# Performance work log

Hardware: AMD Instinct MI355X
Metric: run time of the kernel (lower is better)

The kernel has to match this reference:

```python
import jax, jax.numpy as jnp
import numpy as np

NUM_BINS = 23
SIGMA_RATIO = 0.5
SMOOTH_NR = 1e-07
SMOOTH_DR = 1e-07

BIN_CENTERS = jnp.linspace(0.0, 1.0, NUM_BINS)  # [bins]
_sigma = jnp.mean(BIN_CENTERS[1:] - BIN_CENTERS[:-1]) * SIGMA_RATIO
PRETERM = 1.0 / (2.0 * _sigma ** 2)


def setup_inputs() -> dict:
    key = jax.random.key(0)
    k1, k2 = jax.random.split(key)
    shape = (4, 1, 96, 96, 96)
    pred = jax.random.uniform(k1, shape, dtype=jnp.float32)
    target = jax.random.uniform(k2, shape, dtype=jnp.float32)
    return {"pred": pred, "target": target}


def _parzen(img):
    # img: [B, ...] -> weight [B, N, bins], probability [B, 1, bins]
    img = jnp.clip(img, 0.0, 1.0)
    img = img.reshape(img.shape[0], -1, 1)  # [B, N, 1]
    weight = jnp.exp(-PRETERM * (img - BIN_CENTERS[None, None, :]) ** 2)  # [B, N, bins]
    weight = weight / jnp.sum(weight, axis=-1, keepdims=True)
    probability = jnp.mean(weight, axis=-2, keepdims=True)  # [B, 1, bins]
    return weight, probability


def reference(pred, target):
    wa, pa = _parzen(pred)    # wa: [B, N, bins]
    wb, pb = _parzen(target)
    n = wa.shape[1]
    # joint histogram: [B, bins, bins]
    pab = jnp.einsum('bni,bnj->bij', wa, wb) / n
    # marginal product: [B, bins, bins]
    papb = jnp.einsum('bki,bkj->bij', pa, pb)
    mi = jnp.sum(pab * jnp.log((pab + SMOOTH_NR) / (papb + SMOOTH_DR) + SMOOTH_DR), axis=(1, 2))
    return -jnp.mean(mi)
```

## Files before the change

kernel.cpp:

```cpp
#include <hip/hip_runtime.h>
#include <math.h>


#define NBINS   23
#define NCELLS  529
#define NBATCH  4
#define NVOX    884736
#define PBLK    432
#define RPB     16
#define RBLK    (PBLK / RPB)
#define RS      72
#define IMGB    (32 * RS * 2)
#define WREG    (2 * IMGB)

typedef float    vf4  __attribute__((ext_vector_type(4)));
typedef _Float16 h8   __attribute__((ext_vector_type(8)));
typedef float    f16v __attribute__((ext_vector_type(16)));

#define G1 0.13533528f
#define G2 3.3546263e-4f
#define G3 1.5229979e-8f

__device__ __forceinline__ float window7(float x, int& i0, float* w)
{
    x = fminf(fmaxf(x, 0.0f), 1.0f);
    int ka = (int)floorf(fmaf(x, 22.0f, 0.5f));
    i0 = min(max(ka - 3, 0), 16);
    float v  = fmaf((float)(i0 + 3), -(1.0f / 22.0f), x);
    float W0 = __expf(-968.0f * v * v);
    float R  = __expf(88.0f * v);
    float Ri = __builtin_amdgcn_rcpf(R);
    float R2 = R * R,   R3 = R2 * R;
    float R2i = Ri * Ri, R3i = R2i * Ri;
    w[0] = W0 * (R3i * G3);
    w[1] = W0 * (R2i * G2);
    w[2] = W0 * (Ri  * G1);
    w[3] = W0;
    w[4] = W0 * (R   * G1);
    w[5] = W0 * (R2  * G2);
    w[6] = W0 * (R3  * G3);
    return ((w[0] + w[6]) + (w[1] + w[5])) + ((w[2] + w[4]) + w[3]);
}

__global__ __launch_bounds__(256)
void mi_mfma(const float* __restrict__ pred,
             const float* __restrict__ targ,
             float* __restrict__ partial)
{
    __shared__ __align__(16) char smem[4 * WREG];

    const int p    = blockIdx.x;
    const int b    = blockIdx.y;
    const int wv   = threadIdx.x >> 6;
    const int lane = threadIdx.x & 63;
    const int m    = lane & 31;
    const int h    = lane >> 5;

    char* wbase = smem + wv * WREG;
    _Float16* Aimg = (_Float16*)wbase;
    _Float16* Bimg = (_Float16*)(wbase + IMGB);

    const size_t base = (size_t)b * NVOX + (size_t)p * 2048 + (size_t)wv * 512
                      + (size_t)lane * 8;
    const vf4* __restrict__ px4 = (const vf4*)(pred + base);
    const vf4* __restrict__ py4 = (const vf4*)(targ + base);
    vf4 xa = px4[0], xb = px4[1], ya = py4[0], yb = py4[1];
    float xs[8] = {xa.x, xa.y, xa.z, xa.w, xb.x, xb.y, xb.z, xb.w};
    float ys[8] = {ya.x, ya.y, ya.z, ya.w, yb.x, yb.y, yb.z, yb.w};

    f16v acc = {};

    #pragma unroll
    for (int c = 0; c < 8; ++c) {
        vf4 z = {0.f, 0.f, 0.f, 0.f};
        #pragma unroll
        for (int it = 0; it < 3; ++it) {
            *(vf4*)(wbase        + (it * 64 + lane) * 16) = z;
            *(vf4*)(wbase + IMGB + (it * 64 + lane) * 16) = z;
        }
        if (lane < 24) {
            *(vf4*)(wbase        + (192 + lane) * 16) = z;
            *(vf4*)(wbase + IMGB + (192 + lane) * 16) = z;
        }

        int ia, ja;
        float wa[7], wb[7];
        float sa = window7(xs[c], ia, wa);
        float sb = window7(ys[c], ja, wb);
        float inv = __builtin_amdgcn_rcpf(sa * sb);

        #pragma unroll
        for (int t = 0; t < 7; ++t) {
            Aimg[(ia + t) * RS + lane] = (_Float16)(wa[t] * inv);
            Bimg[(ja + t) * RS + lane] = (_Float16)wb[t];
        }

        #pragma unroll
        for (int s = 0; s < 4; ++s) {
            h8 Af = *(const h8*)(Aimg + m * RS + 16 * s + 8 * h);
            h8 Bf = *(const h8*)(Bimg + m * RS + 16 * s + 8 * h);
            acc = __builtin_amdgcn_mfma_f32_32x32x16_f16(Af, Bf, acc, 0, 0, 0);
        }
    }

    float* tile = (float*)wbase;
    #pragma unroll
    for (int r = 0; r < 16; ++r) {
        int row = (r & 3) + 8 * (r >> 2) + 4 * h;
        tile[row * 33 + m] = acc[r];
    }
    __syncthreads();
    for (int c = threadIdx.x; c < NCELLS; c += 256) {
        int i = c / NBINS, j = c % NBINS;
        float s = 0.0f;
        #pragma unroll
        for (int w = 0; w < 4; ++w)
            s += ((const float*)(smem + w * WREG))[i * 33 + j];
        partial[((size_t)(b * PBLK + p)) * NCELLS + c] = s;
    }
}

__global__ __launch_bounds__(256)
void mi_reduce(const float* __restrict__ partial, double* __restrict__ pab64)
{
    const int g = blockIdx.x;
    const int b = blockIdx.y;
    const int t = threadIdx.x;
    const float* __restrict__ src =
        partial + ((size_t)b * PBLK + (size_t)g * RPB) * NCELLS;

    double a0 = 0.0, a1 = 0.0, a2 = 0.0;
    #pragma unroll
    for (int p = 0; p < RPB; ++p) {
        const float* __restrict__ row = src + (size_t)p * NCELLS;
        a0 += (double)row[t];
        a1 += (double)row[256 + t];
        if (t < NCELLS - 512) a2 += (double)row[512 + t];
    }
    atomicAdd(&pab64[b * NCELLS + t],       a0);
    atomicAdd(&pab64[b * NCELLS + 256 + t], a1);
    if (t < NCELLS - 512) atomicAdd(&pab64[b * NCELLS + 512 + t], a2);
}

__global__ __launch_bounds__(256)
void mi_final(const double* __restrict__ pab64, float* __restrict__ out)
{
    __shared__ double s_pab[NCELLS];
    __shared__ double s_pa[NBINS];
    __shared__ double s_pb[NBINS];
    __shared__ double s_red[4];

    double total = 0.0;
    for (int b = 0; b < NBATCH; ++b) {
        for (int c = threadIdx.x; c < NCELLS; c += 256)
            s_pab[c] = pab64[b * NCELLS + c] * (1.0 / (double)NVOX);
        __syncthreads();
        if (threadIdx.x < NBINS) {
            const int i = threadIdx.x;
            double r = 0.0, cl = 0.0;
            for (int j = 0; j < NBINS; ++j) {
                r  += s_pab[i * NBINS + j];
                cl += s_pab[j * NBINS + i];
            }
            s_pa[i] = r; s_pb[i] = cl;
        }
        __syncthreads();
        double t = 0.0;
        for (int c = threadIdx.x; c < NCELLS; c += 256) {
            double pv   = s_pab[c];
            double papb = s_pa[c / NBINS] * s_pb[c % NBINS];
            t += pv * log((pv + 1e-7) / (papb + 1e-7) + 1e-7);
        }
        #pragma unroll
        for (int off = 32; off > 0; off >>= 1) t += __shfl_down(t, off, 64);
        if ((threadIdx.x & 63) == 0) s_red[threadIdx.x >> 6] = t;
        __syncthreads();
        if (threadIdx.x == 0) total += s_red[0] + s_red[1] + s_red[2] + s_red[3];
        __syncthreads();
    }
    if (threadIdx.x == 0) out[0] = (float)(-total * 0.25);
}

extern "C" void kernel_launch(void* const* d_in, const int* in_sizes, int n_in,
                              void* d_out, int out_size, void* d_ws, size_t ws_size,
                              hipStream_t stream)
{
    const float* pred = (const float*)d_in[0];
    const float* targ = (const float*)d_in[1];
    float* out = (float*)d_out;
    char* ws = (char*)d_ws;

    const size_t off_partial = 0;
    const size_t off_pab64   =
        ((size_t)NBATCH * PBLK * NCELLS * 4 + 255) & ~(size_t)255;

    float*  partial = (float*)(ws + off_partial);
    double* pab64   = (double*)(ws + off_pab64);

    (void)hipMemsetAsync(pab64, 0, (size_t)NBATCH * NCELLS * sizeof(double), stream);
    mi_mfma  <<<dim3(PBLK, NBATCH), 256, 0, stream>>>(pred, targ, partial);
    mi_reduce<<<dim3(RBLK, NBATCH), 256, 0, stream>>>(partial, pab64);
    mi_final <<<1, 256, 0, stream>>>(pab64, out);
}
```

Baseline: 108.8 us.

## Fuse MI histogram, reduction and finalize into one kernel with f64 atomics

Merges the three kernels into one. Each block adds its 529-cell partial histogram straight into a global f64 histogram with hardware atomics, and the last block to finish, detected through a global counter, computes the final MI value. This removes the partial-histogram buffer round trip and two extra launches. Per-wave LDS images also shrink from 32 to 24 rows, and a min-blocks launch bound is added, to allow higher occupancy. The cost is heavy atomic contention: 432 blocks add to each cell per batch. The MFMA fragments now read rows 24 to 31 from neighbouring regions, but only into output entries that are discarded.

```diff
diff --git a/kernel.cpp b/kernel.cpp
--- a/kernel.cpp
+++ b/kernel.cpp
@@ -7,11 +7,11 @@
 #define NBATCH  4
 #define NVOX    884736
 #define PBLK    432
-#define RPB     16
-#define RBLK    (PBLK / RPB)
+#define TOTALB  (PBLK * NBATCH)
 #define RS      72
-#define IMGB    (32 * RS * 2)
+#define IMGB    (24 * RS * 2)
 #define WREG    (2 * IMGB)
+#define SMEMB   (4 * WREG + 2048)
 
 typedef float    vf4  __attribute__((ext_vector_type(4)));
 typedef _Float16 h8   __attribute__((ext_vector_type(8)));
@@ -42,12 +42,20 @@
     return ((w[0] + w[6]) + (w[1] + w[5])) + ((w[2] + w[4]) + w[3]);
 }
 
-__global__ __launch_bounds__(256)
-void mi_mfma(const float* __restrict__ pred,
-             const float* __restrict__ targ,
-             float* __restrict__ partial)
+__device__ __forceinline__ void atomic_add_f64(double* p, double v)
 {
-    __shared__ __align__(16) char smem[4 * WREG];
+    asm volatile("global_atomic_add_f64 %0, %1, off" :: "v"(p), "v"(v) : "memory");
+}
+
+__global__ __launch_bounds__(256, 5)
+void mi_fused(const float* __restrict__ pred,
+              const float* __restrict__ targ,
+              double* __restrict__ pab64,
+              int* __restrict__ counter,
+              float* __restrict__ out)
+{
+    __shared__ __align__(16) char smem[SMEMB];
+    __shared__ int s_last;
 
     const int p    = blockIdx.x;
     const int b    = blockIdx.y;
@@ -74,14 +82,10 @@
     for (int c = 0; c < 8; ++c) {
         vf4 z = {0.f, 0.f, 0.f, 0.f};
         #pragma unroll
-        for (int it = 0; it < 3; ++it) {
-            *(vf4*)(wbase        + (it * 64 + lane) * 16) = z;
-            *(vf4*)(wbase + IMGB + (it * 64 + lane) * 16) = z;
-        }
-        if (lane < 24) {
-            *(vf4*)(wbase        + (192 + lane) * 16) = z;
-            *(vf4*)(wbase + IMGB + (192 + lane) * 16) = z;
-        }
+        for (int it = 0; it < 6; ++it)
+            *(vf4*)(wbase + (it * 64 + lane) * 16) = z;
+        if (lane < 48)
+            *(vf4*)(wbase + (384 + lane) * 16) = z;
 
         int ia, ja;
         float wa[7], wb[7];
@@ -110,50 +114,37 @@
         tile[row * 33 + m] = acc[r];
     }
     __syncthreads();
+    double* dst = pab64 + (size_t)b * NCELLS;
     for (int c = threadIdx.x; c < NCELLS; c += 256) {
         int i = c / NBINS, j = c % NBINS;
         float s = 0.0f;
         #pragma unroll
         for (int w = 0; w < 4; ++w)
             s += ((const float*)(smem + w * WREG))[i * 33 + j];
-        partial[((size_t)(b * PBLK + p)) * NCELLS + c] = s;
+        atomic_add_f64(&dst[c], (double)s);
     }
-}
 
-__global__ __launch_bounds__(256)
-void mi_reduce(const float* __restrict__ partial, double* __restrict__ pab64)
-{
-    const int g = blockIdx.x;
-    const int b = blockIdx.y;
-    const int t = threadIdx.x;
-    const float* __restrict__ src =
-        partial + ((size_t)b * PBLK + (size_t)g * RPB) * NCELLS;
+    __syncthreads();
+    if (threadIdx.x == 0) {
+        __threadfence();
+        int old = atomicAdd(counter, 1);
+        s_last = (old == TOTALB - 1);
+    }
+    __syncthreads();
+    if (!s_last) return;
 
-    double a0 = 0.0, a1 = 0.0, a2 = 0.0;
-    #pragma unroll
-    for (int p = 0; p < RPB; ++p) {
-        const float* __restrict__ row = src + (size_t)p * NCELLS;
-        a0 += (double)row[t];
-        a1 += (double)row[256 + t];
-        if (t < NCELLS - 512) a2 += (double)row[512 + t];
-    }
-    atomicAdd(&pab64[b * NCELLS + t],       a0);
-    atomicAdd(&pab64[b * NCELLS + 256 + t], a1);
-    if (t < NCELLS - 512) atomicAdd(&pab64[b * NCELLS + 512 + t], a2);
-}
-
-__global__ __launch_bounds__(256)
-void mi_final(const double* __restrict__ pab64, float* __restrict__ out)
-{
-    __shared__ double s_pab[NCELLS];
-    __shared__ double s_pa[NBINS];
-    __shared__ double s_pb[NBINS];
-    __shared__ double s_red[4];
+    double* s_pab = (double*)smem;
+    double* s_pa  = (double*)(smem + 4240);
+    double* s_pb  = (double*)(smem + 4432);
+    double* s_red = (double*)(smem + 4624);
 
     double total = 0.0;
-    for (int b = 0; b < NBATCH; ++b) {
+    for (int bb = 0; bb < NBATCH; ++bb) {
         for (int c = threadIdx.x; c < NCELLS; c += 256)
-            s_pab[c] = pab64[b * NCELLS + c] * (1.0 / (double)NVOX);
+            s_pab[c] = __hip_atomic_load(&pab64[bb * NCELLS + c],
+                                         __ATOMIC_RELAXED,
+                                         __HIP_MEMORY_SCOPE_AGENT)
+                       * (1.0 / (double)NVOX);
         __syncthreads();
         if (threadIdx.x < NBINS) {
             const int i = threadIdx.x;
@@ -190,15 +181,9 @@
     float* out = (float*)d_out;
     char* ws = (char*)d_ws;
 
-    const size_t off_partial = 0;
-    const size_t off_pab64   =
-        ((size_t)NBATCH * PBLK * NCELLS * 4 + 255) & ~(size_t)255;
+    double* pab64  = (double*)ws;
+    int*    counter = (int*)(ws + 17024);
 
-    float*  partial = (float*)(ws + off_partial);
-    double* pab64   = (double*)(ws + off_pab64);
-
-    (void)hipMemsetAsync(pab64, 0, (size_t)NBATCH * NCELLS * sizeof(double), stream);
-    mi_mfma  <<<dim3(PBLK, NBATCH), 256, 0, stream>>>(pred, targ, partial);
-    mi_reduce<<<dim3(RBLK, NBATCH), 256, 0, stream>>>(partial, pab64);
-    mi_final <<<1, 256, 0, stream>>>(pab64, out);
+    (void)hipMemsetAsync(ws, 0, 17152, stream);
+    mi_fused<<<dim3(PBLK, NBATCH), 256, 0, stream>>>(pred, targ, pab64, counter, out);
 }
```

After: 128.4 us. 18.0% more time.
